# Performance work log

Hardware: AMD Instinct MI355X
Metric: run time of the kernel (lower is better)

## Reference

```python
import jax, jax.numpy as jnp
import numpy as np

B, S = 128, 1024
IN_NUM, IN_STATE = 64, 16
FEAT = 256
HID = 512
NUM_CLS = 32
EMB_WORD, EMB_DIM = 32, 4
LN_EPS = 1e-5


def _layer_norm(x):
    mu = jnp.mean(x, axis=-1, keepdims=True)
    var = jnp.var(x, axis=-1, keepdims=True)
    return (x - mu) * jax.lax.rsqrt(var + LN_EPS)


def setup_inputs() -> dict:
    key = jax.random.key(0)
    ks = jax.random.split(key, 20)
    w = lambda k, shape: jax.random.normal(k, shape, dtype=jnp.float32) * 0.05
    inp = {
        'x_num': jax.random.normal(ks[0], (B, S, IN_NUM), dtype=jnp.float32),
        'x_state': jax.random.randint(ks[1], (B, S, IN_STATE), 0, EMB_WORD),
        # numeric-branch MLP (2 layers)
        'num_w0': w(ks[2], (FEAT, IN_NUM)), 'num_b0': jnp.zeros((FEAT,), jnp.float32),
        'num_w1': w(ks[3], (FEAT, FEAT)),   'num_b1': jnp.zeros((FEAT,), jnp.float32),
        # state-branch embedding + MLP
        'emb': w(ks[4], (EMB_WORD, EMB_DIM)),
        'st_w0': w(ks[5], (FEAT, IN_STATE * EMB_DIM)), 'st_b0': jnp.zeros((FEAT,), jnp.float32),
        'st_w1': w(ks[6], (FEAT, FEAT)),               'st_b1': jnp.zeros((FEAT,), jnp.float32),
        # LSTM gate weights: input dim = 2*FEAT
        'Wii': w(ks[7], (HID, 2 * FEAT)),  'Whi': w(ks[8], (HID, HID)),
        'Wif': w(ks[9], (HID, 2 * FEAT)),  'Whf': w(ks[10], (HID, HID)),
        'Wig': w(ks[11], (HID, 2 * FEAT)), 'Whg': w(ks[12], (HID, HID)),
        'Wio': w(ks[13], (HID, 2 * FEAT)), 'Who': w(ks[14], (HID, HID)),
        'Bii': jnp.zeros((HID,), jnp.float32), 'Bhi': jnp.zeros((HID,), jnp.float32),
        'Bif': jnp.zeros((HID,), jnp.float32), 'Bhf': jnp.zeros((HID,), jnp.float32),
        'Big': jnp.zeros((HID,), jnp.float32), 'Bhg': jnp.zeros((HID,), jnp.float32),
        'Bio': jnp.zeros((HID,), jnp.float32), 'Bho': jnp.zeros((HID,), jnp.float32),
        'out_w': w(ks[15], (NUM_CLS, HID)), 'out_b': jnp.zeros((NUM_CLS,), jnp.float32),
    }
    return inp


def _forward(x_num, x_state, num_w0, num_b0, num_w1, num_b1, emb,
             st_w0, st_b0, st_w1, st_b1,
             Wii, Whi, Wif, Whf, Wig, Whg, Wio, Who,
             Bii, Bhi, Bif, Bhf, Big, Bhg, Bio, Bho,
             out_w, out_b):
    b, s = x_num.shape[0], x_num.shape[1]
    # numeric branch: Linear -> relu -> LayerNorm (dropout is identity in eval)
    h = _layer_norm(jax.nn.relu(x_num @ num_w0.T + num_b0))
    h = _layer_norm(jax.nn.relu(h @ num_w1.T + num_b1))
    # state branch: embedding lookup, flatten per step, then MLP
    e = emb[x_state].reshape(b, s, -1)                      # [B,S,IN_STATE*EMB_DIM]
    g = _layer_norm(jax.nn.relu(e @ st_w0.T + st_b0))
    g = _layer_norm(jax.nn.relu(g @ st_w1.T + st_b1))
    x = jnp.concatenate([h, g], axis=2)                     # [B,S,2*FEAT]

    hid = Whi.shape[0]
    h0 = jnp.zeros((b, hid), x.dtype)
    c0 = jnp.zeros((b, hid), x.dtype)

    def step(carry, x_t):
        h_t, c_t = carry
        i_t = jax.nn.sigmoid(x_t @ Wii.T + h_t @ Whi.T + Bii + Bhi)
        f_t = jax.nn.sigmoid(x_t @ Wif.T + h_t @ Whf.T + Bif + Bhf)
        g_t = jnp.tanh(x_t @ Wig.T + h_t @ Whg.T + Big + Bhg)
        o_t = jax.nn.sigmoid(x_t @ Wio.T + h_t @ Who.T + Bio + Bho)
        c_new = f_t * c_t + i_t * g_t
        h_new = o_t * jnp.tanh(c_new)
        return (h_new, c_new), None

    (h_last, _), _ = jax.lax.scan(step, (h0, c0), jnp.swapaxes(x, 0, 1))
    return h_last @ out_w.T + out_b                          # [B, num_cls]


def reference(x_num, x_state, num_w0, num_b0, num_w1, num_b1, emb,
              st_w0, st_b0, st_w1, st_b1,
              Wii, Whi, Wif, Whf, Wig, Whg, Wio, Who,
              Bii, Bhi, Bif, Bhf, Big, Bhg, Bio, Bho,
              out_w, out_b):
    return _forward(x_num, x_state, num_w0, num_b0, num_w1, num_b1, emb,
                    st_w0, st_b0, st_w1, st_b1,
                    Wii, Whi, Wif, Whf, Wig, Whg, Wio, Who,
                    Bii, Bhi, Bif, Bhf, Big, Bhg, Bio, Bho,
                    out_w, out_b)
```

## Files before the change

### kernel.cpp

```cpp
#include <hip/hip_runtime.h>
#include <hip/hip_bf16.h>

typedef __attribute__((ext_vector_type(4))) float f4;
typedef __attribute__((ext_vector_type(4))) float f32x4;
typedef __attribute__((ext_vector_type(8))) short bf16x8;
typedef unsigned long long ull;

#define OFF_XCAT   0ull
#define OFF_WCAT   134217728ull
#define OFF_BIAS   138412032ull
#define OFF_HBUF   138420224ull
#define OFF_FLAG   138682368ull
#define OFF_CTR    138690560ull
#define WS_NEED    138691584ull

__device__ inline unsigned short f2bf(float x){
  unsigned u = __float_as_uint(x);
  unsigned r = (u + 0x7FFFu + ((u >> 16) & 1u)) >> 16;
  return (unsigned short)r;
}
__device__ inline float bf2f(unsigned short s){ return __uint_as_float(((unsigned)s) << 16); }

__global__ void __launch_bounds__(256) diag_write(float* out, float val){
  out[blockIdx.x * 256 + threadIdx.x] = val;
}

__global__ void __launch_bounds__(256) prep_w(
    const float* Wii, const float* Wif, const float* Wig, const float* Wio,
    const float* Whi, const float* Whf, const float* Whg, const float* Who,
    const float* Bii, const float* Bif, const float* Big, const float* Bio,
    const float* Bhi, const float* Bhf, const float* Bhg, const float* Bho,
    unsigned short* Wcat, float* bias_cat){
  int e = blockIdx.x * 256 + threadIdx.x;
  int col = e >> 10, k = e & 1023;
  int u = col >> 2, g = col & 3;
  float v;
  if (k < 512){
    const float* p = (g==0)?Wii:((g==1)?Wif:((g==2)?Wig:Wio));
    v = p[u*512 + k];
  } else {
    const float* p = (g==0)?Whi:((g==1)?Whf:((g==2)?Whg:Who));
    v = p[u*512 + (k-512)];
  }
  Wcat[e] = f2bf(v);
  if (e < 2048){
    int u2 = e >> 2, g2 = e & 3;
    const float* bx = (g2==0)?Bii:((g2==1)?Bif:((g2==2)?Big:Bio));
    const float* bh = (g2==0)?Bhi:((g2==1)?Bhf:((g2==2)?Bhg:Bho));
    bias_cat[e] = bx[u2] + bh[u2];
  }
}

__global__ void __launch_bounds__(256) stageA_fused(
    const float* __restrict__ xnum, const int* __restrict__ xstate,
    const float* __restrict__ emb,
    const float* __restrict__ num_w0, const float* __restrict__ num_b0,
    const float* __restrict__ num_w1, const float* __restrict__ num_b1,
    const float* __restrict__ st_w0,  const float* __restrict__ st_b0,
    const float* __restrict__ st_w1,  const float* __restrict__ st_b1,
    unsigned short* __restrict__ Xcat){
  __shared__ float Wt[32*256];
  __shared__ float xb[16*68];
  __shared__ float h1[16*260];
  int tid = threadIdx.x;
  long tok0 = (long)blockIdx.x * 16;
  int tg = tid >> 6, c4 = tid & 63;

  #pragma unroll 1
  for (int br = 0; br < 2; ++br){
    const float* W0 = br ? st_w0 : num_w0;
    const float* b0 = br ? st_b0 : num_b0;
    const float* W1 = br ? st_w1 : num_w1;
    const float* b1 = br ? st_b1 : num_b1;

    __syncthreads();
    if (br == 0){
      int tk = tid >> 4, q = tid & 15;
      f4 v = *(const f4*)(xnum + (tok0+tk)*64 + q*4);
      float* d = xb + tk*68 + q*4;
      d[0]=v.x; d[1]=v.y; d[2]=v.z; d[3]=v.w;
    } else {
      int tk = tid >> 4, j = tid & 15;
      int idx = xstate[(tok0+tk)*16 + j];
      f4 v = *(const f4*)(emb + idx*4);
      float* d = xb + tk*68 + j*4;
      d[0]=v.x; d[1]=v.y; d[2]=v.z; d[3]=v.w;
    }

    float acc[4][4];
    { f4 bv = *(const f4*)(b0 + c4*4);
      #pragma unroll
      for (int j=0;j<4;j++){ acc[j][0]=bv.x; acc[j][1]=bv.y; acc[j][2]=bv.z; acc[j][3]=bv.w; } }
    for (int kh=0; kh<2; ++kh){
      __syncthreads();
      { int c = tid;
        const f4* src = (const f4*)(W0 + c*64 + kh*32);
        #pragma unroll
        for (int q=0;q<8;q++){
          f4 v = src[q];
          Wt[(q*4+0)*256 + c] = v.x; Wt[(q*4+1)*256 + c] = v.y;
          Wt[(q*4+2)*256 + c] = v.z; Wt[(q*4+3)*256 + c] = v.w;
        }
      }
      __syncthreads();
      for (int kq=0; kq<8; kq++){
        int k0 = kh*32 + kq*4;
        f4 a0 = *(const f4*)(xb + (tg*4+0)*68 + k0);
        f4 a1 = *(const f4*)(xb + (tg*4+1)*68 + k0);
        f4 a2 = *(const f4*)(xb + (tg*4+2)*68 + k0);
        f4 a3 = *(const f4*)(xb + (tg*4+3)*68 + k0);
        f4 w0 = *(const f4*)(Wt + (kq*4+0)*256 + c4*4);
        f4 w1 = *(const f4*)(Wt + (kq*4+1)*256 + c4*4);
        f4 w2 = *(const f4*)(Wt + (kq*4+2)*256 + c4*4);
        f4 w3 = *(const f4*)(Wt + (kq*4+3)*256 + c4*4);
        #pragma unroll
        for (int j=0;j<4;j++){
          f4 a = (j==0)?a0:((j==1)?a1:((j==2)?a2:a3));
          #pragma unroll
          for (int d=0; d<4; d++)
            acc[j][d] += a.x*w0[d] + a.y*w1[d] + a.z*w2[d] + a.w*w3[d];
        }
      }
    }
    #pragma unroll
    for (int j=0;j<4;j++){
      float v0=fmaxf(acc[j][0],0.f), v1=fmaxf(acc[j][1],0.f);
      float v2=fmaxf(acc[j][2],0.f), v3=fmaxf(acc[j][3],0.f);
      float s1 = v0+v1+v2+v3, s2 = v0*v0+v1*v1+v2*v2+v3*v3;
      for (int off=1; off<64; off<<=1){ s1 += __shfl_xor(s1, off); s2 += __shfl_xor(s2, off); }
      float mu = s1 * (1.f/256.f);
      float rs = rsqrtf(s2*(1.f/256.f) - mu*mu + 1e-5f);
      f4 o; o.x=(v0-mu)*rs; o.y=(v1-mu)*rs; o.z=(v2-mu)*rs; o.w=(v3-mu)*rs;
      *(f4*)(h1 + (tg*4+j)*260 + c4*4) = o;
    }

    float ac2[4][4];
    { f4 bv = *(const f4*)(b1 + c4*4);
      #pragma unroll
      for (int j=0;j<4;j++){ ac2[j][0]=bv.x; ac2[j][1]=bv.y; ac2[j][2]=bv.z; ac2[j][3]=bv.w; } }
    for (int kh=0; kh<8; ++kh){
      __syncthreads();
      { int c = tid;
        const f4* src = (const f4*)(W1 + c*256 + kh*32);
        #pragma unroll
        for (int q=0;q<8;q++){
          f4 v = src[q];
          Wt[(q*4+0)*256 + c] = v.x; Wt[(q*4+1)*256 + c] = v.y;
          Wt[(q*4+2)*256 + c] = v.z; Wt[(q*4+3)*256 + c] = v.w;
        }
      }
      __syncthreads();
      for (int kq=0; kq<8; kq++){
        int k0 = kh*32 + kq*4;
        f4 a0 = *(const f4*)(h1 + (tg*4+0)*260 + k0);
        f4 a1 = *(const f4*)(h1 + (tg*4+1)*260 + k0);
        f4 a2 = *(const f4*)(h1 + (tg*4+2)*260 + k0);
        f4 a3 = *(const f4*)(h1 + (tg*4+3)*260 + k0);
        f4 w0 = *(const f4*)(Wt + (kq*4+0)*256 + c4*4);
        f4 w1 = *(const f4*)(Wt + (kq*4+1)*256 + c4*4);
        f4 w2 = *(const f4*)(Wt + (kq*4+2)*256 + c4*4);
        f4 w3 = *(const f4*)(Wt + (kq*4+3)*256 + c4*4);
        #pragma unroll
        for (int j=0;j<4;j++){
          f4 a = (j==0)?a0:((j==1)?a1:((j==2)?a2:a3));
          #pragma unroll
          for (int d=0; d<4; d++)
            ac2[j][d] += a.x*w0[d] + a.y*w1[d] + a.z*w2[d] + a.w*w3[d];
        }
      }
    }
    #pragma unroll
    for (int j=0;j<4;j++){
      float v0=fmaxf(ac2[j][0],0.f), v1=fmaxf(ac2[j][1],0.f);
      float v2=fmaxf(ac2[j][2],0.f), v3=fmaxf(ac2[j][3],0.f);
      float s1 = v0+v1+v2+v3, s2 = v0*v0+v1*v1+v2*v2+v3*v3;
      for (int off=1; off<64; off<<=1){ s1 += __shfl_xor(s1, off); s2 += __shfl_xor(s2, off); }
      float mu = s1 * (1.f/256.f);
      float rs = rsqrtf(s2*(1.f/256.f) - mu*mu + 1e-5f);
      long tok = tok0 + tg*4 + j;
      long bb = tok >> 10, ss = tok & 1023;
      unsigned short* o = Xcat + (ss*128 + bb)*512 + br*256 + c4*4;
      unsigned lo = (unsigned)f2bf((v0-mu)*rs) | ((unsigned)f2bf((v1-mu)*rs) << 16);
      unsigned hi = (unsigned)f2bf((v2-mu)*rs) | ((unsigned)f2bf((v3-mu)*rs) << 16);
      ((unsigned*)o)[0] = lo; ((unsigned*)o)[1] = hi;
    }
  }
}

__global__ void __launch_bounds__(256, 1) lstm_pk(
    const unsigned short* __restrict__ Xcat,
    const unsigned short* __restrict__ Wcat,
    const float* __restrict__ bias_cat,
    unsigned int* __restrict__ hbuf32,
    ull* __restrict__ flg,
    unsigned int* __restrict__ ctr){
  __shared__ __align__(16) char actb[32768];
  __shared__ int okf, sdead;
  int tid = threadIdx.x;
  int lane = tid & 63, w = tid >> 6;
  int g = blockIdx.x & 7, m = blockIdx.x >> 3;

  int colg = 64*m + 16*w + (lane & 15);
  bf16x8 wf[32];
  {
    const bf16x8* wsrc = (const bf16x8*)(Wcat + colg*1024 + (lane>>4)*8);
    #pragma unroll
    for (int s=0;s<32;s++) wf[s] = wsrc[s*4];
    #pragma unroll
    for (int s=0;s<32;s++) asm volatile("" : "+v"(wf[s]));
  }
  int cb = 64*m + 16*w + 4*(lane>>4);
  f32x4 bias4;
  bias4.x = bias_cat[cb+0]; bias4.y = bias_cat[cb+1];
  bias4.z = bias_cat[cb+2]; bias4.w = bias_cat[cb+3];

  if (tid == 0){
    __hip_atomic_fetch_add(&ctr[255], 1u, __ATOMIC_RELAXED, __HIP_MEMORY_SCOPE_AGENT);
    unsigned v = 0; int it = 0;
    do {
      v = __hip_atomic_load(&ctr[255], __ATOMIC_RELAXED, __HIP_MEMORY_SCOPE_AGENT);
      if (v >= 256u) break;
      __builtin_amdgcn_s_sleep(8);
    } while (++it < 2000000);
    okf = (v >= 256u) ? 1 : 0;
    sdead = 0;
  }
  __syncthreads();
  if (!okf) return;

  float cst = 0.f;
  int r16 = tid >> 4, q16 = tid & 15;
  ull* f8 = flg + g*128;
  unsigned int* myflag = (unsigned int*)(f8 + (m*4 + w));

  f32x4 acc0, acc1;
  {
    bf16x8 xf[16];
    const bf16x8* xsrc = (const bf16x8*)(Xcat + ((long)0*128 + g*16 + (lane&15))*512 + (lane>>4)*8);
    #pragma unroll
    for (int s=0;s<16;s++) xf[s] = xsrc[s*4];
    acc0 = bias4;
    acc1.x=0.f; acc1.y=0.f; acc1.z=0.f; acc1.w=0.f;
    #pragma unroll
    for (int s=0;s<16;s+=2){
      acc0 = __builtin_amdgcn_mfma_f32_16x16x32_bf16(wf[s],   xf[s],   acc0, 0, 0, 0);
      acc1 = __builtin_amdgcn_mfma_f32_16x16x32_bf16(wf[s+1], xf[s+1], acc1, 0, 0, 0);
    }
  }

  #pragma unroll 1
  for (int t=0; t<1024; ++t){
    if (t > 0){
      unsigned tt = (unsigned)t; int itc = 0;
      for (;;){
        unsigned a = __hip_atomic_load((const unsigned int*)(f8 + lane),      __ATOMIC_RELAXED, __HIP_MEMORY_SCOPE_AGENT);
        unsigned b = __hip_atomic_load((const unsigned int*)(f8 + 64 + lane), __ATOMIC_RELAXED, __HIP_MEMORY_SCOPE_AGENT);
        if (__all((int)(a >= tt)) && __all((int)(b >= tt))) break;
        if ((itc & 127) == 127 && *(volatile int*)&sdead) break;
        if (++itc > 400000){
          *(volatile int*)&sdead = 1;
          __hip_atomic_store(&ctr[252], tt, __ATOMIC_RELAXED, __HIP_MEMORY_SCOPE_AGENT);
          break;
        }
      }
      asm volatile("" ::: "memory");
    }
    {
      const ull* hb = (const ull*)hbuf32 + ((long)(t&1)*8 + g)*(16*128) + r16*128 + q16;
      ull hv[8];
      #pragma unroll
      for (int i=0;i<8;i++)
        hv[i] = __hip_atomic_load(&hb[i*16], __ATOMIC_RELAXED, __HIP_MEMORY_SCOPE_AGENT);
      char* hl = actb + (t&1)*16384;
      #pragma unroll
      for (int i=0;i<8;i++){
        int byt = (r16*1024 + q16*8 + i*128) ^ ((r16 & 7) << 4);
        *(ull*)(hl + byt) = hv[i];
      }
    }
    __syncthreads();
    if (*(volatile int*)&sdead) break;
    {
      const char* hl = actb + (t&1)*16384;
      #pragma unroll
      for (int s=0;s<16;s+=2){
        int by0 = ((lane&15)*1024 + s*64     + (lane>>4)*16) ^ (((lane&15)&7) << 4);
        int by1 = ((lane&15)*1024 + (s+1)*64 + (lane>>4)*16) ^ (((lane&15)&7) << 4);
        bf16x8 b0 = *(const bf16x8*)(hl + by0);
        bf16x8 b1 = *(const bf16x8*)(hl + by1);
        acc0 = __builtin_amdgcn_mfma_f32_16x16x32_bf16(wf[16+s], b0, acc0, 0, 0, 0);
        acc1 = __builtin_amdgcn_mfma_f32_16x16x32_bf16(wf[17+s], b1, acc1, 0, 0, 0);
      }
    }
    float gi = acc0.x + acc1.x, gf = acc0.y + acc1.y;
    float gg = acc0.z + acc1.z, go = acc0.w + acc1.w;
    float iv = 1.f / (1.f + __expf(-gi));
    float fv = 1.f / (1.f + __expf(-gf));
    float e2 = __expf(-2.f * gg);
    float gv = (1.f - e2) / (1.f + e2);
    float ov = 1.f / (1.f + __expf(-go));
    cst = fv * cst + iv * gv;
    float e2c = __expf(-2.f * cst);
    float hout = ov * (1.f - e2c) / (1.f + e2c);
    {
      unsigned short hb16 = f2bf(hout);
      int partner = __shfl_xor((int)hb16, 16);
      int hi = lane >> 4;
      if ((hi & 1) == 0){
        int ug = 16*m + 4*w + hi;
        int r = lane & 15;
        unsigned pack = (unsigned)hb16 | (((unsigned)partner & 0xFFFFu) << 16);
        unsigned int* dst = hbuf32 + ((long)((t+1)&1)*8 + g)*(16*256) + r*256 + (ug >> 1);
        __hip_atomic_store(dst, pack, __ATOMIC_RELAXED, __HIP_MEMORY_SCOPE_AGENT);
      }
    }
    asm volatile("s_waitcnt vmcnt(0)" ::: "memory");
    if (lane == 0)
      __hip_atomic_store(myflag, (unsigned)(t+1), __ATOMIC_RELAXED, __HIP_MEMORY_SCOPE_AGENT);
    {
      int tn = (t < 1023) ? (t+1) : 1023;
      bf16x8 xf[16];
      const bf16x8* xsrc = (const bf16x8*)(Xcat + ((long)tn*128 + g*16 + (lane&15))*512 + (lane>>4)*8);
      #pragma unroll
      for (int s=0;s<16;s++) xf[s] = xsrc[s*4];
      acc0 = bias4;
      acc1.x=0.f; acc1.y=0.f; acc1.z=0.f; acc1.w=0.f;
      #pragma unroll
      for (int s=0;s<16;s+=2){
        acc0 = __builtin_amdgcn_mfma_f32_16x16x32_bf16(wf[s],   xf[s],   acc0, 0, 0, 0);
        acc1 = __builtin_amdgcn_mfma_f32_16x16x32_bf16(wf[s+1], xf[s+1], acc1, 0, 0, 0);
      }
    }
  }

  __syncthreads();
  if (tid == 0 && !sdead)
    __hip_atomic_fetch_add(&ctr[251], 1u, __ATOMIC_RELAXED, __HIP_MEMORY_SCOPE_AGENT);
}

__global__ void __launch_bounds__(256) out_gemm(
    const unsigned short* __restrict__ hbuf, const unsigned int* __restrict__ ctr,
    const float* __restrict__ out_w, const float* __restrict__ out_b,
    float* __restrict__ out){
  unsigned done = ctr[251], arriv = ctr[255], dead = ctr[252];
  if (dead != 0u || done != 256u){
    float v = dead ? (20000.f + (float)dead) : (10000.f + (float)arriv);
    if (threadIdx.x < 32) out[blockIdx.x*32 + threadIdx.x] = v;
    return;
  }
  __shared__ float part[8][32];
  int b = blockIdx.x;
  int g = b >> 4, r = b & 15;
  const unsigned short* hrow = hbuf + ((long)g*16 + r)*512;
  int col = threadIdx.x & 31, p = threadIdx.x >> 5;
  float s = 0.f;
  for (int u = p*64; u < p*64 + 64; ++u)
    s += bf2f(hrow[u]) * out_w[col*512 + u];
  part[p][col] = s;
  __syncthreads();
  if (p == 0){
    float t = out_b[col];
    #pragma unroll
    for (int i=0;i<8;i++) t += part[i][col];
    out[b*32 + col] = t;
  }
}

extern "C" void kernel_launch(void* const* d_in, const int* in_sizes, int n_in,
                              void* d_out, int out_size, void* d_ws, size_t ws_size,
                              hipStream_t stream){
  const float* x_num   = (const float*)d_in[0];
  const int*   x_state = (const int*)d_in[1];
  const float* num_w0  = (const float*)d_in[2];
  const float* num_b0  = (const float*)d_in[3];
  const float* num_w1  = (const float*)d_in[4];
  const float* num_b1  = (const float*)d_in[5];
  const float* emb     = (const float*)d_in[6];
  const float* st_w0   = (const float*)d_in[7];
  const float* st_b0   = (const float*)d_in[8];
  const float* st_w1   = (const float*)d_in[9];
  const float* st_b1   = (const float*)d_in[10];
  const float* Wii = (const float*)d_in[11];
  const float* Whi = (const float*)d_in[12];
  const float* Wif = (const float*)d_in[13];
  const float* Whf = (const float*)d_in[14];
  const float* Wig = (const float*)d_in[15];
  const float* Whg = (const float*)d_in[16];
  const float* Wio = (const float*)d_in[17];
  const float* Who = (const float*)d_in[18];
  const float* Bii = (const float*)d_in[19];
  const float* Bhi = (const float*)d_in[20];
  const float* Bif = (const float*)d_in[21];
  const float* Bhf = (const float*)d_in[22];
  const float* Big = (const float*)d_in[23];
  const float* Bhg = (const float*)d_in[24];
  const float* Bio = (const float*)d_in[25];
  const float* Bho = (const float*)d_in[26];
  const float* out_w = (const float*)d_in[27];
  const float* out_b = (const float*)d_in[28];

  float* out = (float*)d_out;

  diag_write<<<16, 256, 0, stream>>>(out, 50000.f);

  if (ws_size < WS_NEED){
    diag_write<<<16, 256, 0, stream>>>(out, 100000.f + (float)(ws_size >> 20));
    return;
  }

  char* ws = (char*)d_ws;
  unsigned short* Xcat = (unsigned short*)(ws + OFF_XCAT);
  unsigned short* Wcat = (unsigned short*)(ws + OFF_WCAT);
  float* bias_cat      = (float*)(ws + OFF_BIAS);
  unsigned int* hbuf32 = (unsigned int*)(ws + OFF_HBUF);
  ull* flg             = (ull*)(ws + OFF_FLAG);
  unsigned int* ctr    = (unsigned int*)(ws + OFF_CTR);

  hipMemsetAsync(ws + OFF_HBUF, 0, 262144 + 8192 + 1024, stream);

  prep_w<<<8192, 256, 0, stream>>>(Wii, Wif, Wig, Wio, Whi, Whf, Whg, Who,
                                   Bii, Bif, Big, Bio, Bhi, Bhf, Bhg, Bho,
                                   Wcat, bias_cat);

  stageA_fused<<<8192, 256, 0, stream>>>(x_num, x_state, emb,
                                         num_w0, num_b0, num_w1, num_b1,
                                         st_w0, st_b0, st_w1, st_b1, Xcat);

  lstm_pk<<<256, 256, 0, stream>>>(Xcat, Wcat, bias_cat, hbuf32, flg, ctr);

  out_gemm<<<128, 256, 0, stream>>>((const unsigned short*)hbuf32, ctr, out_w, out_b, out);
}
```

Before: 5.467 ms.

## Embed step tags in h words to replace flag polling, move Wh to LDS

```diff
diff --git a/kernel.cpp b/kernel.cpp
--- a/kernel.cpp
+++ b/kernel.cpp
@@ -9,10 +9,9 @@
 #define OFF_XCAT   0ull
 #define OFF_WCAT   134217728ull
 #define OFF_BIAS   138412032ull
-#define OFF_HBUF   138420224ull
-#define OFF_FLAG   138682368ull
-#define OFF_CTR    138690560ull
-#define WS_NEED    138691584ull
+#define OFF_HW     138420224ull
+#define OFF_CTR    138944512ull
+#define WS_NEED    138945536ull
 
 __device__ inline unsigned short f2bf(float x){
   unsigned u = __float_as_uint(x);
@@ -191,23 +190,34 @@
     const unsigned short* __restrict__ Xcat,
     const unsigned short* __restrict__ Wcat,
     const float* __restrict__ bias_cat,
-    unsigned int* __restrict__ hbuf32,
-    ull* __restrict__ flg,
+    unsigned int* __restrict__ hw,
     unsigned int* __restrict__ ctr){
   __shared__ __align__(16) char actb[32768];
+  extern __shared__ __align__(16) char wlds[];
   __shared__ int okf, sdead;
   int tid = threadIdx.x;
   int lane = tid & 63, w = tid >> 6;
   int g = blockIdx.x & 7, m = blockIdx.x >> 3;
 
+  #pragma unroll
+  for (int i=0;i<16;i++){
+    int c16 = tid + (i<<8);
+    int ww  = c16 >> 10;
+    int col = (c16 >> 6) & 15;
+    int kc  = c16 & 63;
+    const bf16x8* src = (const bf16x8*)(Wcat + (long)(64*m + 16*ww + col)*1024 + 512 + kc*8);
+    int off = ((ww<<14) + (col<<10) + (kc<<4)) ^ ((col & 7) << 4);
+    *(bf16x8*)(wlds + off) = *src;
+  }
+
   int colg = 64*m + 16*w + (lane & 15);
-  bf16x8 wf[32];
+  bf16x8 wfx[16];
   {
-    const bf16x8* wsrc = (const bf16x8*)(Wcat + colg*1024 + (lane>>4)*8);
-    #pragma unroll
-    for (int s=0;s<32;s++) wf[s] = wsrc[s*4];
-    #pragma unroll
-    for (int s=0;s<32;s++) asm volatile("" : "+v"(wf[s]));
+    const bf16x8* wsrc = (const bf16x8*)(Wcat + (long)colg*1024 + (lane>>4)*8);
+    #pragma unroll
+    for (int s=0;s<16;s++) wfx[s] = wsrc[s*4];
+    #pragma unroll
+    for (int s=0;s<16;s++) asm volatile("" : "+v"(wfx[s]));
   }
   int cb = 64*m + 16*w + 4*(lane>>4);
   f32x4 bias4;
@@ -230,8 +240,8 @@
 
   float cst = 0.f;
   int r16 = tid >> 4, q16 = tid & 15;
-  ull* f8 = flg + g*128;
-  unsigned int* myflag = (unsigned int*)(f8 + (m*4 + w));
+  int wbase = (w<<14) + ((lane&15)<<10);
+  int wswz  = ((lane&15)&7)<<4;
 
   f32x4 acc0, acc1;
   {
@@ -243,39 +253,46 @@
     acc1.x=0.f; acc1.y=0.f; acc1.z=0.f; acc1.w=0.f;
     #pragma unroll
     for (int s=0;s<16;s+=2){
-      acc0 = __builtin_amdgcn_mfma_f32_16x16x32_bf16(wf[s],   xf[s],   acc0, 0, 0, 0);
-      acc1 = __builtin_amdgcn_mfma_f32_16x16x32_bf16(wf[s+1], xf[s+1], acc1, 0, 0, 0);
+      acc0 = __builtin_amdgcn_mfma_f32_16x16x32_bf16(wfx[s],   xf[s],   acc0, 0, 0, 0);
+      acc1 = __builtin_amdgcn_mfma_f32_16x16x32_bf16(wfx[s+1], xf[s+1], acc1, 0, 0, 0);
     }
   }
 
   #pragma unroll 1
   for (int t=0; t<1024; ++t){
-    if (t > 0){
-      unsigned tt = (unsigned)t; int itc = 0;
-      for (;;){
-        unsigned a = __hip_atomic_load((const unsigned int*)(f8 + lane),      __ATOMIC_RELAXED, __HIP_MEMORY_SCOPE_AGENT);
-        unsigned b = __hip_atomic_load((const unsigned int*)(f8 + 64 + lane), __ATOMIC_RELAXED, __HIP_MEMORY_SCOPE_AGENT);
-        if (__all((int)(a >= tt)) && __all((int)(b >= tt))) break;
-        if ((itc & 127) == 127 && *(volatile int*)&sdead) break;
-        if (++itc > 400000){
-          *(volatile int*)&sdead = 1;
-          __hip_atomic_store(&ctr[252], tt, __ATOMIC_RELAXED, __HIP_MEMORY_SCOPE_AGENT);
-          break;
+    {
+      const unsigned int* hp = hw + ((long)(t&1)*65536) + g*8192 + r16*512 + q16*32;
+      unsigned hv[32];
+      if (t > 0){
+        unsigned tt = (unsigned)t & 0xFFFFu; int itc = 0;
+        for (;;){
+          #pragma unroll
+          for (int i=0;i<32;i++)
+            hv[i] = __hip_atomic_load(&hp[i], __ATOMIC_RELAXED, __HIP_MEMORY_SCOPE_AGENT);
+          unsigned bad = 0;
+          #pragma unroll
+          for (int i=0;i<32;i++) bad |= (hv[i] & 0xFFFFu) ^ tt;
+          if (!bad) break;
+          if ((itc & 31) == 31 && *(volatile int*)&sdead) break;
+          if (++itc > 100000){
+            *(volatile int*)&sdead = 1;
+            __hip_atomic_store(&ctr[252], (unsigned)t, __ATOMIC_RELAXED, __HIP_MEMORY_SCOPE_AGENT);
+            break;
+          }
         }
-      }
-      asm volatile("" ::: "memory");
-    }
-    {
-      const ull* hb = (const ull*)hbuf32 + ((long)(t&1)*8 + g)*(16*128) + r16*128 + q16;
-      ull hv[8];
-      #pragma unroll
-      for (int i=0;i<8;i++)
-        hv[i] = __hip_atomic_load(&hb[i*16], __ATOMIC_RELAXED, __HIP_MEMORY_SCOPE_AGENT);
+      } else {
+        #pragma unroll
+        for (int i=0;i<32;i++)
+          hv[i] = __hip_atomic_load(&hp[i], __ATOMIC_RELAXED, __HIP_MEMORY_SCOPE_AGENT);
+      }
       char* hl = actb + (t&1)*16384;
       #pragma unroll
       for (int i=0;i<8;i++){
-        int byt = (r16*1024 + q16*8 + i*128) ^ ((r16 & 7) << 4);
-        *(ull*)(hl + byt) = hv[i];
+        unsigned p0 = (hv[4*i+0] >> 16) | (hv[4*i+1] & 0xFFFF0000u);
+        unsigned p1 = (hv[4*i+2] >> 16) | (hv[4*i+3] & 0xFFFF0000u);
+        ull pp = (ull)p0 | ((ull)p1 << 32);
+        int byt = (r16*1024 + q16*64 + i*8) ^ ((r16 & 7) << 4);
+        *(ull*)(hl + byt) = pp;
       }
     }
     __syncthreads();
@@ -284,12 +301,14 @@
       const char* hl = actb + (t&1)*16384;
       #pragma unroll
       for (int s=0;s<16;s+=2){
-        int by0 = ((lane&15)*1024 + s*64     + (lane>>4)*16) ^ (((lane&15)&7) << 4);
-        int by1 = ((lane&15)*1024 + (s+1)*64 + (lane>>4)*16) ^ (((lane&15)&7) << 4);
+        bf16x8 wb0 = *(const bf16x8*)(wlds + ((wbase + s*64     + ((lane>>4)<<4)) ^ wswz));
+        bf16x8 wb1 = *(const bf16x8*)(wlds + ((wbase + (s+1)*64 + ((lane>>4)<<4)) ^ wswz));
+        int by0 = (((lane&15)<<10) + s*64     + ((lane>>4)<<4)) ^ wswz;
+        int by1 = (((lane&15)<<10) + (s+1)*64 + ((lane>>4)<<4)) ^ wswz;
         bf16x8 b0 = *(const bf16x8*)(hl + by0);
         bf16x8 b1 = *(const bf16x8*)(hl + by1);
-        acc0 = __builtin_amdgcn_mfma_f32_16x16x32_bf16(wf[16+s], b0, acc0, 0, 0, 0);
-        acc1 = __builtin_amdgcn_mfma_f32_16x16x32_bf16(wf[17+s], b1, acc1, 0, 0, 0);
+        acc0 = __builtin_amdgcn_mfma_f32_16x16x32_bf16(wb0, b0, acc0, 0, 0, 0);
+        acc1 = __builtin_amdgcn_mfma_f32_16x16x32_bf16(wb1, b1, acc1, 0, 0, 0);
       }
     }
     float gi = acc0.x + acc1.x, gf = acc0.y + acc1.y;
@@ -304,19 +323,12 @@
     float hout = ov * (1.f - e2c) / (1.f + e2c);
     {
       unsigned short hb16 = f2bf(hout);
-      int partner = __shfl_xor((int)hb16, 16);
-      int hi = lane >> 4;
-      if ((hi & 1) == 0){
-        int ug = 16*m + 4*w + hi;
-        int r = lane & 15;
-        unsigned pack = (unsigned)hb16 | (((unsigned)partner & 0xFFFFu) << 16);
-        unsigned int* dst = hbuf32 + ((long)((t+1)&1)*8 + g)*(16*256) + r*256 + (ug >> 1);
-        __hip_atomic_store(dst, pack, __ATOMIC_RELAXED, __HIP_MEMORY_SCOPE_AGENT);
-      }
-    }
-    asm volatile("s_waitcnt vmcnt(0)" ::: "memory");
-    if (lane == 0)
-      __hip_atomic_store(myflag, (unsigned)(t+1), __ATOMIC_RELAXED, __HIP_MEMORY_SCOPE_AGENT);
+      int unit = 16*m + 4*w + (lane >> 4);
+      int row  = lane & 15;
+      unsigned word = ((unsigned)hb16 << 16) | ((unsigned)(t+1) & 0xFFFFu);
+      unsigned int* dst = hw + ((long)((t+1)&1)*65536) + g*8192 + row*512 + unit;
+      __hip_atomic_store(dst, word, __ATOMIC_RELAXED, __HIP_MEMORY_SCOPE_AGENT);
+    }
     {
       int tn = (t < 1023) ? (t+1) : 1023;
       bf16x8 xf[16];
@@ -327,8 +339,8 @@
       acc1.x=0.f; acc1.y=0.f; acc1.z=0.f; acc1.w=0.f;
       #pragma unroll
       for (int s=0;s<16;s+=2){
-        acc0 = __builtin_amdgcn_mfma_f32_16x16x32_bf16(wf[s],   xf[s],   acc0, 0, 0, 0);
-        acc1 = __builtin_amdgcn_mfma_f32_16x16x32_bf16(wf[s+1], xf[s+1], acc1, 0, 0, 0);
+        acc0 = __builtin_amdgcn_mfma_f32_16x16x32_bf16(wfx[s],   xf[s],   acc0, 0, 0, 0);
+        acc1 = __builtin_amdgcn_mfma_f32_16x16x32_bf16(wfx[s+1], xf[s+1], acc1, 0, 0, 0);
       }
     }
   }
@@ -339,7 +351,7 @@
 }
 
 __global__ void __launch_bounds__(256) out_gemm(
-    const unsigned short* __restrict__ hbuf, const unsigned int* __restrict__ ctr,
+    const unsigned int* __restrict__ hw, const unsigned int* __restrict__ ctr,
     const float* __restrict__ out_w, const float* __restrict__ out_b,
     float* __restrict__ out){
   unsigned done = ctr[251], arriv = ctr[255], dead = ctr[252];
@@ -351,11 +363,11 @@
   __shared__ float part[8][32];
   int b = blockIdx.x;
   int g = b >> 4, r = b & 15;
-  const unsigned short* hrow = hbuf + ((long)g*16 + r)*512;
+  const unsigned int* hrow = hw + (long)g*8192 + r*512;
   int col = threadIdx.x & 31, p = threadIdx.x >> 5;
   float s = 0.f;
   for (int u = p*64; u < p*64 + 64; ++u)
-    s += bf2f(hrow[u]) * out_w[col*512 + u];
+    s += bf2f((unsigned short)(hrow[u] >> 16)) * out_w[col*512 + u];
   part[p][col] = s;
   __syncthreads();
   if (p == 0){
@@ -412,11 +424,10 @@
   unsigned short* Xcat = (unsigned short*)(ws + OFF_XCAT);
   unsigned short* Wcat = (unsigned short*)(ws + OFF_WCAT);
   float* bias_cat      = (float*)(ws + OFF_BIAS);
-  unsigned int* hbuf32 = (unsigned int*)(ws + OFF_HBUF);
-  ull* flg             = (ull*)(ws + OFF_FLAG);
+  unsigned int* hw     = (unsigned int*)(ws + OFF_HW);
   unsigned int* ctr    = (unsigned int*)(ws + OFF_CTR);
 
-  hipMemsetAsync(ws + OFF_HBUF, 0, 262144 + 8192 + 1024, stream);
+  hipMemsetAsync(ws + OFF_HW, 0, 524288 + 1024, stream);
 
   prep_w<<<8192, 256, 0, stream>>>(Wii, Wif, Wig, Wio, Whi, Whf, Whg, Who,
                                    Bii, Bif, Big, Bio, Bhi, Bhf, Bhg, Bho,
@@ -426,7 +437,9 @@
                                          num_w0, num_b0, num_w1, num_b1,
                                          st_w0, st_b0, st_w1, st_b1, Xcat);
 
-  lstm_pk<<<256, 256, 0, stream>>>(Xcat, Wcat, bias_cat, hbuf32, flg, ctr);
-
-  out_gemm<<<128, 256, 0, stream>>>((const unsigned short*)hbuf32, ctr, out_w, out_b, out);
-}
+  hipFuncSetAttribute((const void*)lstm_pk,
+                      hipFuncAttributeMaxDynamicSharedMemorySize, 65536);
+  lstm_pk<<<256, 256, 65536, stream>>>(Xcat, Wcat, bias_cat, hw, ctr);
+
+  out_gemm<<<128, 256, 0, stream>>>(hw, ctr, out_w, out_b, out);
+}
```

After: 12.32 ms. +125.4%, slower.
